# Optimization experiments

Hardware: AMD Instinct MI355X
Metric: run time of the kernel (lower is better)

## Reference

```python
import jax, jax.numpy as jnp
import numpy as np

B, S, E, H = 8, 2048, 1024, 64

def setup_inputs() -> dict:
    key = jax.random.key(0)
    ks = jax.random.split(key, 7)
    scale = 1.0 / np.sqrt(E)
    return {
        "x": jax.random.normal(ks[0], (B, S, E), dtype=jnp.float32),
        "mask": jnp.ones((B, S), dtype=jnp.int32),
        "Wq": jax.random.uniform(ks[1], (E, H), jnp.float32, -scale, scale),
        "bq": jax.random.uniform(ks[2], (H,), jnp.float32, -scale, scale),
        "Wk": jax.random.uniform(ks[3], (E, H), jnp.float32, -scale, scale),
        "bk": jax.random.uniform(ks[4], (H,), jnp.float32, -scale, scale),
        "Wv": jax.random.uniform(ks[5], (E, H), jnp.float32, -scale, scale),
        "bv": jax.random.uniform(ks[6], (H,), jnp.float32, -scale, scale),
    }

def reference(x, mask, Wq, bq, Wk, bk, Wv, bv):
    # q,k,v: [B,S,H]
    q = jnp.einsum('bse,eh->bsh', x, Wq) + bq
    k = jnp.einsum('bse,eh->bsh', x, Wk) + bk
    v = jnp.einsum('bse,eh->bsh', x, Wv) + bv
    # scores: [B,S,S]
    scores = jnp.einsum('bqh,bkh->bqk', q, k) / jnp.sqrt(jnp.asarray(H, q.dtype))
    causal = jnp.tril(jnp.ones((S, S), dtype=bool))  # [S,S]
    pad = (mask != 0)[:, None, :]                    # [B,1,S]
    neg_inf = jnp.asarray(float('-inf'), scores.dtype)
    scores = jnp.where(causal[None] & pad, scores, neg_inf)
    attn = jax.nn.softmax(scores, axis=-1)
    return jnp.einsum('bqk,bkh->bqh', attn, v)
```

## Files before the change

kernel.cpp:

```cpp
#include <hip/hip_runtime.h>
#include <hip/hip_bf16.h>

#define S_ 2048
#define E_ 1024
#define QNC 32

typedef __attribute__((ext_vector_type(8))) short short8;
typedef __attribute__((ext_vector_type(4))) float f32x4;

__device__ __forceinline__ short f2bf(float f) {
    __hip_bfloat16 h = __float2bfloat16(f);
    return *(short*)&h;
}

__device__ __forceinline__ void g2l16(const void* g, void* l) {
    __builtin_amdgcn_global_load_lds(
        (const __attribute__((address_space(1))) void*)g,
        (__attribute__((address_space(3))) void*)l, 16, 0, 0);
}

__global__ __launch_bounds__(256) void prep_weights(
    const float* __restrict__ Wq, const float* __restrict__ Wk,
    const float* __restrict__ Wv, unsigned short* __restrict__ Wt)
{
    int idx = blockIdx.x * 256 + threadIdx.x;
    int n = idx >> 10, k = idx & (E_ - 1);
    const float* W = (n < 64) ? Wq : (n < 128) ? Wk : Wv;
    Wt[idx] = (unsigned short)f2bf(W[k * 64 + (n & 63)]);
}

__global__ __launch_bounds__(256, 4) void qkv_main(
    const float* __restrict__ x, const unsigned short* __restrict__ Wt,
    const float* __restrict__ bq, const float* __restrict__ bk,
    const float* __restrict__ bv,
    unsigned short* __restrict__ Q, unsigned short* __restrict__ K,
    unsigned short* __restrict__ Vt)
{
    __shared__ __align__(16) char pool[2][14336];
    int tid = threadIdx.x;
    int wave = tid >> 6, lane = tid & 63;
    int lo = lane & 15, hi = lane >> 4;
    int wn = wave;
    int rowbase = blockIdx.x * 16;
    const char* xg = (const char*)x;
    const char* wg = (const char*)Wt;

    f32x4 acc[3];
    #pragma unroll
    for (int j = 0; j < 3; ++j) acc[j] = (f32x4){0.f, 0.f, 0.f, 0.f};

    #define STAGE(bb, kc)                                                         \
        {                                                                         \
            if (tid < 128) {                                                      \
                int r = tid >> 3, u = tid & 7;                                    \
                const char* src = xg + (size_t)(rowbase + r) * 4096 + (kc) * 128  \
                                  + ((u ^ (r & 7)) << 4);                         \
                g2l16(src, &pool[bb][wave * 1024]);                               \
            }                                                                     \
            _Pragma("unroll")                                                     \
            for (int i = 0; i < 3; ++i) {                                         \
                int w_ = i * 256 + tid;                                           \
                int cl = w_ >> 2, u = w_ & 3;                                     \
                const char* src = wg + (size_t)cl * 2048 + (kc) * 64              \
                                  + ((u ^ ((cl ^ (cl >> 2)) & 3)) << 4);          \
                g2l16(src, &pool[bb][2048 + (i * 256 + wave * 64) * 16]);         \
            }                                                                     \
        }

    STAGE(0, 0);
    asm volatile("s_waitcnt vmcnt(0)" ::: "memory");
    __builtin_amdgcn_sched_barrier(0);
    __builtin_amdgcn_s_barrier();

    for (int t = 0; t < QNC; ++t) {
        if (t + 1 < QNC) STAGE((t + 1) & 1, t + 1);

        const char* lx = pool[t & 1];
        const char* lw = pool[t & 1] + 2048;

        short8 bf[3];
        #pragma unroll
        for (int j = 0; j < 3; ++j) {
            int cl = wn * 48 + j * 16 + lo;
            bf[j] = *(const short8*)(lw + cl * 64
                + ((hi ^ ((cl ^ (cl >> 2)) & 3)) << 4));
        }
        {
            int r = lo;
            int u0 = 2 * hi;
            float4 a0 = *(const float4*)(lx + r * 128 + ((u0 ^ (r & 7)) << 4));
            float4 a1 = *(const float4*)(lx + r * 128 + (((u0 + 1) ^ (r & 7)) << 4));
            short8 af;
            af[0] = f2bf(a0.x); af[1] = f2bf(a0.y);
            af[2] = f2bf(a0.z); af[3] = f2bf(a0.w);
            af[4] = f2bf(a1.x); af[5] = f2bf(a1.y);
            af[6] = f2bf(a1.z); af[7] = f2bf(a1.w);
            #pragma unroll
            for (int j = 0; j < 3; ++j)
                acc[j] = __builtin_amdgcn_mfma_f32_16x16x32_bf16(af, bf[j], acc[j], 0, 0, 0);
        }

        __builtin_amdgcn_sched_barrier(0);
        asm volatile("s_waitcnt vmcnt(0)" ::: "memory");
        __builtin_amdgcn_sched_barrier(0);
        __builtin_amdgcn_s_barrier();
    }
    #undef STAGE

    __syncthreads();
    char* eq = pool[0];
    unsigned short* ev = (unsigned short*)pool[1];
    #pragma unroll
    for (int j = 0; j < 3; ++j) {
        int n = wn * 48 + j * 16 + lo;
        #pragma unroll
        for (int r4 = 0; r4 < 4; ++r4) {
            int rr = 4 * hi + r4;
            float v = acc[j][r4];
            if (n < 64) {
                *(unsigned short*)(eq + rr * 272 + n * 2) =
                    (unsigned short)f2bf(v + bq[n]);
            } else if (n < 128) {
                *(unsigned short*)(eq + rr * 272 + n * 2) =
                    (unsigned short)f2bf(v + bk[n - 64]);
            } else {
                ev[(n - 128) * 18 + rr] = (unsigned short)f2bf(v + bv[n - 128]);
            }
        }
    }
    __syncthreads();

    {
        int row = tid >> 4, seg = tid & 15;
        short8 val = *(const short8*)(eq + row * 272 + seg * 16);
        if (seg < 8)
            *(short8*)(Q + (size_t)(rowbase + row) * 64 + seg * 8) = val;
        else
            *(short8*)(K + (size_t)(rowbase + row) * 64 + (seg - 8) * 8) = val;
    }
    if (tid < 128) {
        int h = tid >> 1, su = tid & 1;
        int b = rowbase >> 11, sl0 = rowbase & (S_ - 1);
        short8 val = *(const short8*)((const char*)ev + h * 36 + su * 16);
        *(short8*)(Vt + ((size_t)(b * 64 + h)) * S_ + sl0 + su * 8) = val;
    }
}

__global__ __launch_bounds__(256) void attn_stage(
    const unsigned short* __restrict__ Q, const unsigned short* __restrict__ K,
    const unsigned short* __restrict__ Vt, const int* __restrict__ mask,
    float* __restrict__ part)
{
    __shared__ __align__(16) char kv[3][16384];
    __shared__ __align__(16) unsigned short p_lds[4][16][72];
    int tid = threadIdx.x;
    int wave = tid >> 6, lane = tid & 63;
    int lo = lane & 15, hi = lane >> 4;
    int blk = blockIdx.x;
    int c = blk & 3;
    int pr = blk >> 2;
    int b = pr & 7;
    int qt64 = 31 - (pr >> 3);
    int nkt = qt64 + 1;
    int chunk = (nkt + 3) >> 2;
    int kt0 = c * chunk;
    int kt1 = min(kt0 + chunk, nkt);
    int ntile = kt1 - kt0;
    int qrow0 = qt64 * 64 + wave * 16;

    f32x4 o[4];
    float ps[4] = {0.f, 0.f, 0.f, 0.f};
    #pragma unroll
    for (int i = 0; i < 4; ++i) o[i] = (f32x4){0.f, 0.f, 0.f, 0.f};

    #define ASTAGE(bb, kt)                                                        \
        {                                                                         \
            int kbase_ = (kt) * 64;                                               \
            const char* kg = (const char*)K + (size_t)(b * S_ + kbase_) * 128;    \
            const char* vg = (const char*)Vt + (size_t)b * 64 * 4096 + kbase_ * 2;\
            _Pragma("unroll")                                                     \
            for (int j = 0; j < 2; ++j) {                                         \
                int r = (j * 4 + wave) * 8 + (lane >> 3);                         \
                int un = lane & 7;                                                \
                g2l16(kg + r * 128 + ((un ^ (r & 7)) << 4),                       \
                      &kv[bb][(j * 4 + wave) * 1024]);                            \
                g2l16(vg + (size_t)r * 4096 + ((un ^ (r & 7)) << 4),              \
                      &kv[bb][8192 + (j * 4 + wave) * 1024]);                     \
            }                                                                     \
        }

    if (ntile > 0) {
        const unsigned short* qp = Q + ((size_t)(b * S_ + qrow0 + lo)) * 64 + 8 * hi;
        short8 qf0 = *(const short8*)(qp);
        short8 qf1 = *(const short8*)(qp + 32);

        unsigned mbits = 0;
        for (int tt = 0; tt < 8; ++tt) {
            if (tt < ntile) {
                int kbase = (kt0 + tt) * 64;
                #pragma unroll
                for (int nt = 0; nt < 4; ++nt)
                    if (mask[b * S_ + kbase + nt * 16 + lo] != 0)
                        mbits |= (1u << (tt * 4 + nt));
            }
        }
        asm volatile("s_waitcnt vmcnt(0)" ::: "memory");
        __builtin_amdgcn_sched_barrier(0);

        ASTAGE(0, kt0);
        if (ntile > 1) ASTAGE(1, kt0 + 1);
        __builtin_amdgcn_sched_barrier(0);
        if (ntile > 1) asm volatile("s_waitcnt vmcnt(4)" ::: "memory");
        else           asm volatile("s_waitcnt vmcnt(0)" ::: "memory");
        __builtin_amdgcn_sched_barrier(0);
        __builtin_amdgcn_s_barrier();

        for (int t = 0; t < ntile; ++t) {
            int kbase = (kt0 + t) * 64;
            const char* kb = kv[t % 3];
            const char* vb = kv[t % 3] + 8192;

            f32x4 s[4];
            #pragma unroll
            for (int i = 0; i < 4; ++i) s[i] = (f32x4){0.f, 0.f, 0.f, 0.f};
            #pragma unroll
            for (int nt = 0; nt < 4; ++nt) {
                short8 kf0 = *(const short8*)(kb + (nt * 16 + lo) * 128 + ((hi ^ (lo & 7)) << 4));
                short8 kf1 = *(const short8*)(kb + (nt * 16 + lo) * 128 + (((4 + hi) ^ (lo & 7)) << 4));
                s[nt] = __builtin_amdgcn_mfma_f32_16x16x32_bf16(qf0, kf0, s[nt], 0, 0, 0);
                s[nt] = __builtin_amdgcn_mfma_f32_16x16x32_bf16(qf1, kf1, s[nt], 0, 0, 0);
            }

            #pragma unroll
            for (int nt = 0; nt < 4; ++nt) {
                int kpos = kbase + nt * 16 + lo;
                bool mok = (mbits >> (t * 4 + nt)) & 1;
                #pragma unroll
                for (int r = 0; r < 4; ++r) {
                    int qpos = qrow0 + 4 * hi + r;
                    bool ok = mok && (kpos <= qpos);
                    float pv = ok ? __expf(s[nt][r] * 0.125f) : 0.f;
                    ps[r] += pv;
                    p_lds[wave][4 * hi + r][nt * 16 + lo] = (unsigned short)f2bf(pv);
                }
            }

            #pragma unroll
            for (int kk = 0; kk < 2; ++kk) {
                short8 pf = *(const short8*)&p_lds[wave][lo][kk * 32 + 8 * hi];
                #pragma unroll
                for (int nt = 0; nt < 4; ++nt) {
                    short8 vf = *(const short8*)(vb + (nt * 16 + lo) * 128
                                                 + (((kk * 4 + hi) ^ (lo & 7)) << 4));
                    o[nt] = __builtin_amdgcn_mfma_f32_16x16x32_bf16(pf, vf, o[nt], 0, 0, 0);
                }
            }

            if (t + 2 < ntile) ASTAGE((t + 2) % 3, kt0 + t + 2);
            __builtin_amdgcn_sched_barrier(0);
            if (t + 1 < ntile) {
                if (t + 2 < ntile) asm volatile("s_waitcnt vmcnt(4)" ::: "memory");
                else               asm volatile("s_waitcnt vmcnt(0)" ::: "memory");
                __builtin_amdgcn_sched_barrier(0);
                __builtin_amdgcn_s_barrier();
            }
        }
    }
    #undef ASTAGE

    float l[4];
    #pragma unroll
    for (int r = 0; r < 4; ++r) {
        float v = ps[r];
        v += __shfl_xor(v, 1);
        v += __shfl_xor(v, 2);
        v += __shfl_xor(v, 4);
        v += __shfl_xor(v, 8);
        l[r] = v;
    }

    int tile16 = b * 128 + qt64 * 4 + wave;
    float* pp = part + (((size_t)c * 1024 + tile16) * 64 + lane) * 20;
    #pragma unroll
    for (int nt = 0; nt < 4; ++nt) *(f32x4*)(pp + nt * 4) = o[nt];
    f32x4 ll;
    #pragma unroll
    for (int r = 0; r < 4; ++r) ll[r] = l[r];
    *(f32x4*)(pp + 16) = ll;
}

__global__ __launch_bounds__(256) void attn_comb(
    const float* __restrict__ part, float* __restrict__ out)
{
    int g = blockIdx.x * 256 + threadIdx.x;
    int tile = g >> 6, lane = g & 63;
    int lo = lane & 15, hi = lane >> 4;
    int b = tile >> 7, qt = tile & 127;
    int qrow0 = qt * 16;

    f32x4 o[4];
    float l[4] = {0.f, 0.f, 0.f, 0.f};
    #pragma unroll
    for (int i = 0; i < 4; ++i) o[i] = (f32x4){0.f, 0.f, 0.f, 0.f};

    #pragma unroll
    for (int c = 0; c < 4; ++c) {
        const float* pp = part + (((size_t)c * 1024 + tile) * 64 + lane) * 20;
        #pragma unroll
        for (int nt = 0; nt < 4; ++nt) {
            f32x4 po = *(const f32x4*)(pp + nt * 4);
            #pragma unroll
            for (int r = 0; r < 4; ++r) o[nt][r] += po[r];
        }
        f32x4 pl = *(const f32x4*)(pp + 16);
        #pragma unroll
        for (int r = 0; r < 4; ++r) l[r] += pl[r];
    }

    #pragma unroll
    for (int nt = 0; nt < 4; ++nt) {
        #pragma unroll
        for (int r = 0; r < 4; ++r) {
            int qpos = qrow0 + 4 * hi + r;
            out[((size_t)(b * S_ + qpos)) * 64 + nt * 16 + lo] =
                (l[r] > 0.f) ? o[nt][r] / l[r] : 0.f;
        }
    }
}

extern "C" void kernel_launch(void* const* d_in, const int* in_sizes, int n_in,
                              void* d_out, int out_size, void* d_ws, size_t ws_size,
                              hipStream_t stream) {
    const float* x   = (const float*)d_in[0];
    const int*   msk = (const int*)d_in[1];
    const float* Wq  = (const float*)d_in[2];
    const float* bq  = (const float*)d_in[3];
    const float* Wk  = (const float*)d_in[4];
    const float* bk  = (const float*)d_in[5];
    const float* Wv  = (const float*)d_in[6];
    const float* bv  = (const float*)d_in[7];
    float* outp = (float*)d_out;

    char* w = (char*)d_ws;
    unsigned short* Wt = (unsigned short*)w;
    unsigned short* Qb = (unsigned short*)(w + 0x080000);
    unsigned short* Kb = (unsigned short*)(w + 0x280000);
    unsigned short* Vt = (unsigned short*)(w + 0x480000);
    float* partp = (float*)(w + 0x680000);

    prep_weights<<<dim3(768), dim3(256), 0, stream>>>(Wq, Wk, Wv, Wt);
    qkv_main<<<dim3(1024), dim3(256), 0, stream>>>(x, Wt, bq, bk, bv, Qb, Kb, Vt);
    attn_stage<<<dim3(1024), dim3(256), 0, stream>>>(Qb, Kb, Vt, msk, partp);
    attn_comb<<<dim3(256), dim3(256), 0, stream>>>(partp, outp);
}
```

Measured before the change: 66.50 us.

## Pre-swizzle weights into MFMA fragment layout and drop LDS staging in QKV projection

The weight prep kernel now writes W in a per-lane MFMA B-fragment order, so qkv_main can load fragments straight from global memory. This removes the LDS double-buffered staging and the per-step barriers. qkv_main now uses 512-thread blocks covering 32 rows, with two row-groups of waves sharing the weight fragments, and launches half as many blocks. The trade-off is that x and W reads now come from global memory with no LDS reuse, so performance leans on cache hits and on load latency being hidden.

Measured after the change: 81.53 us. +22.6%, slower.

```diff
diff --git a/kernel.cpp b/kernel.cpp
--- a/kernel.cpp
+++ b/kernel.cpp
@@ -3,7 +3,6 @@
 
 #define S_ 2048
 #define E_ 1024
-#define QNC 32
 
 typedef __attribute__((ext_vector_type(8))) short short8;
 typedef __attribute__((ext_vector_type(4))) float f32x4;
@@ -21,101 +20,65 @@
 
 __global__ __launch_bounds__(256) void prep_weights(
     const float* __restrict__ Wq, const float* __restrict__ Wk,
-    const float* __restrict__ Wv, unsigned short* __restrict__ Wt)
+    const float* __restrict__ Wv, unsigned short* __restrict__ Wtt)
 {
-    int idx = blockIdx.x * 256 + threadIdx.x;
-    int n = idx >> 10, k = idx & (E_ - 1);
+    int tw = blockIdx.x * 256 + threadIdx.x;
+    int nt = tw >> 11;
+    int lane = tw & 63;
+    int n = nt * 16 + (lane & 15);
+    int h = n & 63;
     const float* W = (n < 64) ? Wq : (n < 128) ? Wk : Wv;
-    Wt[idx] = (unsigned short)f2bf(W[k * 64 + (n & 63)]);
-}
-
-__global__ __launch_bounds__(256, 4) void qkv_main(
-    const float* __restrict__ x, const unsigned short* __restrict__ Wt,
+    int k0 = ((tw >> 6) & 31) * 32 + (lane >> 4) * 8;
+    short8 o;
+    #pragma unroll
+    for (int e = 0; e < 8; ++e) o[e] = f2bf(W[(k0 + e) * 64 + h]);
+    *(short8*)(Wtt + (size_t)tw * 8) = o;
+}
+
+__global__ __launch_bounds__(512, 2) void qkv_main(
+    const float* __restrict__ x, const unsigned short* __restrict__ Wtt,
     const float* __restrict__ bq, const float* __restrict__ bk,
     const float* __restrict__ bv,
     unsigned short* __restrict__ Q, unsigned short* __restrict__ K,
     unsigned short* __restrict__ Vt)
 {
-    __shared__ __align__(16) char pool[2][14336];
+    __shared__ __align__(16) char eq[32 * 272];
+    __shared__ __align__(16) unsigned short ev[64 * 40];
     int tid = threadIdx.x;
     int wave = tid >> 6, lane = tid & 63;
     int lo = lane & 15, hi = lane >> 4;
-    int wn = wave;
-    int rowbase = blockIdx.x * 16;
-    const char* xg = (const char*)x;
-    const char* wg = (const char*)Wt;
+    int wm = wave >> 2, wn = wave & 3;
+    int rowbase = blockIdx.x * 32;
 
     f32x4 acc[3];
     #pragma unroll
     for (int j = 0; j < 3; ++j) acc[j] = (f32x4){0.f, 0.f, 0.f, 0.f};
 
-    #define STAGE(bb, kc)                                                         \
-        {                                                                         \
-            if (tid < 128) {                                                      \
-                int r = tid >> 3, u = tid & 7;                                    \
-                const char* src = xg + (size_t)(rowbase + r) * 4096 + (kc) * 128  \
-                                  + ((u ^ (r & 7)) << 4);                         \
-                g2l16(src, &pool[bb][wave * 1024]);                               \
-            }                                                                     \
-            _Pragma("unroll")                                                     \
-            for (int i = 0; i < 3; ++i) {                                         \
-                int w_ = i * 256 + tid;                                           \
-                int cl = w_ >> 2, u = w_ & 3;                                     \
-                const char* src = wg + (size_t)cl * 2048 + (kc) * 64              \
-                                  + ((u ^ ((cl ^ (cl >> 2)) & 3)) << 4);          \
-                g2l16(src, &pool[bb][2048 + (i * 256 + wave * 64) * 16]);         \
-            }                                                                     \
-        }
-
-    STAGE(0, 0);
-    asm volatile("s_waitcnt vmcnt(0)" ::: "memory");
-    __builtin_amdgcn_sched_barrier(0);
-    __builtin_amdgcn_s_barrier();
-
-    for (int t = 0; t < QNC; ++t) {
-        if (t + 1 < QNC) STAGE((t + 1) & 1, t + 1);
-
-        const char* lx = pool[t & 1];
-        const char* lw = pool[t & 1] + 2048;
-
-        short8 bf[3];
+    const float* xr = x + (size_t)(rowbase + wm * 16 + lo) * E_ + 8 * hi;
+    const unsigned short* wp = Wtt + (size_t)(wn * 3) * 32 * 64 * 8 + (size_t)lane * 8;
+
+    #pragma unroll 4
+    for (int ks = 0; ks < 32; ++ks) {
+        float4 a0 = *(const float4*)(xr + ks * 32);
+        float4 a1 = *(const float4*)(xr + ks * 32 + 4);
+        short8 af;
+        af[0] = f2bf(a0.x); af[1] = f2bf(a0.y);
+        af[2] = f2bf(a0.z); af[3] = f2bf(a0.w);
+        af[4] = f2bf(a1.x); af[5] = f2bf(a1.y);
+        af[6] = f2bf(a1.z); af[7] = f2bf(a1.w);
         #pragma unroll
         for (int j = 0; j < 3; ++j) {
-            int cl = wn * 48 + j * 16 + lo;
-            bf[j] = *(const short8*)(lw + cl * 64
-                + ((hi ^ ((cl ^ (cl >> 2)) & 3)) << 4));
-        }
-        {
-            int r = lo;
-            int u0 = 2 * hi;
-            float4 a0 = *(const float4*)(lx + r * 128 + ((u0 ^ (r & 7)) << 4));
-            float4 a1 = *(const float4*)(lx + r * 128 + (((u0 + 1) ^ (r & 7)) << 4));
-            short8 af;
-            af[0] = f2bf(a0.x); af[1] = f2bf(a0.y);
-            af[2] = f2bf(a0.z); af[3] = f2bf(a0.w);
-            af[4] = f2bf(a1.x); af[5] = f2bf(a1.y);
-            af[6] = f2bf(a1.z); af[7] = f2bf(a1.w);
-            #pragma unroll
-            for (int j = 0; j < 3; ++j)
-                acc[j] = __builtin_amdgcn_mfma_f32_16x16x32_bf16(af, bf[j], acc[j], 0, 0, 0);
-        }
-
-        __builtin_amdgcn_sched_barrier(0);
-        asm volatile("s_waitcnt vmcnt(0)" ::: "memory");
-        __builtin_amdgcn_sched_barrier(0);
-        __builtin_amdgcn_s_barrier();
-    }
-    #undef STAGE
-
-    __syncthreads();
-    char* eq = pool[0];
-    unsigned short* ev = (unsigned short*)pool[1];
+            short8 bf = *(const short8*)(wp + ((size_t)j * 32 + ks) * 64 * 8);
+            acc[j] = __builtin_amdgcn_mfma_f32_16x16x32_bf16(af, bf, acc[j], 0, 0, 0);
+        }
+    }
+
     #pragma unroll
     for (int j = 0; j < 3; ++j) {
         int n = wn * 48 + j * 16 + lo;
         #pragma unroll
         for (int r4 = 0; r4 < 4; ++r4) {
-            int rr = 4 * hi + r4;
+            int rr = wm * 16 + 4 * hi + r4;
             float v = acc[j][r4];
             if (n < 64) {
                 *(unsigned short*)(eq + rr * 272 + n * 2) =
@@ -124,7 +87,7 @@
                 *(unsigned short*)(eq + rr * 272 + n * 2) =
                     (unsigned short)f2bf(v + bk[n - 64]);
             } else {
-                ev[(n - 128) * 18 + rr] = (unsigned short)f2bf(v + bv[n - 128]);
+                ev[(n - 128) * 40 + rr] = (unsigned short)f2bf(v + bv[n - 128]);
             }
         }
     }
@@ -138,10 +101,10 @@
         else
             *(short8*)(K + (size_t)(rowbase + row) * 64 + (seg - 8) * 8) = val;
     }
-    if (tid < 128) {
-        int h = tid >> 1, su = tid & 1;
+    if (tid < 256) {
+        int h = tid >> 2, su = tid & 3;
         int b = rowbase >> 11, sl0 = rowbase & (S_ - 1);
-        short8 val = *(const short8*)((const char*)ev + h * 36 + su * 16);
+        short8 val = *(const short8*)(ev + h * 40 + su * 8);
         *(short8*)(Vt + ((size_t)(b * 64 + h)) * S_ + sl0 + su * 8) = val;
     }
 }
@@ -342,14 +305,14 @@
     float* outp = (float*)d_out;
 
     char* w = (char*)d_ws;
-    unsigned short* Wt = (unsigned short*)w;
+    unsigned short* Wtt = (unsigned short*)w;
     unsigned short* Qb = (unsigned short*)(w + 0x080000);
     unsigned short* Kb = (unsigned short*)(w + 0x280000);
     unsigned short* Vt = (unsigned short*)(w + 0x480000);
     float* partp = (float*)(w + 0x680000);
 
-    prep_weights<<<dim3(768), dim3(256), 0, stream>>>(Wq, Wk, Wv, Wt);
-    qkv_main<<<dim3(1024), dim3(256), 0, stream>>>(x, Wt, bq, bk, bv, Qb, Kb, Vt);
+    prep_weights<<<dim3(96), dim3(256), 0, stream>>>(Wq, Wk, Wv, Wtt);
+    qkv_main<<<dim3(512), dim3(512), 0, stream>>>(x, Wtt, bq, bk, bv, Qb, Kb, Vt);
     attn_stage<<<dim3(1024), dim3(256), 0, stream>>>(Qb, Kb, Vt, msk, partp);
     attn_comb<<<dim3(256), dim3(256), 0, stream>>>(partp, outp);
 }
```
